# Kernel tuning notes

Hardware: AMD Instinct MI355X
Metric: run time of the kernel (lower is better)

Reference implementation:

```python
import jax, jax.numpy as jnp
import numpy as np

# Model dims (match init_kwargs)
E = 2048   # embed_dim
H = 16     # num_heads
QR = 512   # q_low_rank
KVR = 512  # kv_low_rank
DR = 64    # rope_dim
DV = 128   # v_head_dim
S = 2048   # seq_len


def _make_rotary(seq_len, dim):
    inv_freq = 1.0 / jnp.power(10000.0, jnp.arange(0, dim, 2, dtype=jnp.float32) / dim)
    t = jnp.arange(seq_len, dtype=jnp.float32)
    freqs = jnp.outer(t, inv_freq)  # (S, dim//2)
    return jnp.sin(freqs), jnp.cos(freqs)


def _apply_rope(x, sin, cos):
    # x: (S, H_or_1, D); sin/cos: (S, D//2)
    d = x.shape[-1] // 2
    x1, x2 = x[..., :d], x[..., d:]
    s = jnp.concatenate([sin, sin], axis=-1)[:, None, :]
    c = jnp.concatenate([cos, cos], axis=-1)[:, None, :]
    return x * c + jnp.concatenate([-x2, x1], axis=-1) * s


def setup_inputs() -> dict:
    key = jax.random.key(0)
    ks = jax.random.split(key, 8)
    def lin(k, out_dim, in_dim):
        return jax.random.normal(k, (out_dim, in_dim), dtype=jnp.float32) * (1.0 / np.sqrt(in_dim))
    return {
        "x": jax.random.normal(ks[0], (S, E), dtype=jnp.float32),
        "wq_down": lin(ks[1], QR, E),
        "wq_up": lin(ks[2], H * DV, QR),
        "wq_rope": lin(ks[3], H * DR, QR),
        "wkv_down": lin(ks[4], KVR, E),
        "wkv_up": lin(ks[5], H * 2 * DV, KVR),
        "wk_rope": lin(ks[6], DR, E),
        "wo": lin(ks[7], E, H * DV),
    }


def reference(x, wq_down, wq_up, wq_rope, wkv_down, wkv_up, wk_rope, wo):
    seq = x.shape[0]
    # Query path: low-rank bottleneck -> content + rope streams
    c_q = x @ wq_down.T                                   # (S, QR)
    q_content = (c_q @ wq_up.T).reshape(seq, H, DV)       # (S, H, DV)
    q_rope = (c_q @ wq_rope.T).reshape(seq, H, DR)        # (S, H, DR)
    # KV path: shared low-rank bottleneck
    c_kv = x @ wkv_down.T                                 # (S, KVR)
    kv = c_kv @ wkv_up.T                                  # (S, 2*H*DV)
    k_content_flat, v_flat = jnp.split(kv, 2, axis=-1)
    k_content = k_content_flat.reshape(seq, H, DV)
    v = v_flat.reshape(seq, H, DV)
    # Shared key-RoPE projection (one per position, broadcast over heads)
    k_rope_shared = (x @ wk_rope.T)[:, None, :]           # (S, 1, DR)
    sin, cos = _make_rotary(seq, DR)
    q_rope_rot = _apply_rope(q_rope, sin, cos)            # (S, H, DR)
    k_rope_rot = _apply_rope(k_rope_shared, sin, cos)     # (S, 1, DR)
    # Concat content + rope streams; QK head dim = DV + DR
    dt = jnp.bfloat16
    q = jnp.concatenate([q_content, q_rope_rot], axis=-1).astype(dt)                            # (S, H, DV+DR)
    k = jnp.concatenate([k_content, jnp.broadcast_to(k_rope_rot, (seq, H, DR))], axis=-1).astype(dt)
    v_attn = v.astype(dt)
    scale = 1.0 / np.sqrt(DV + DR)
    # Attention. Note: original zero-pads V to DV+DR then slices output back to
    # DV -- mathematically identical to attending with unpadded V.
    logits = jnp.einsum('shd,thd->hst', q, k).astype(jnp.float32) * scale  # (H, S, S)
    probs = jax.nn.softmax(logits, axis=-1).astype(dt)
    attn = jnp.einsum('hst,thd->shd', probs, v_attn)      # (S, H, DV)
    attn_flat = attn.reshape(seq, H * DV)
    return (attn_flat @ wo.T).astype(jnp.float32)         # (S, E)
```

## Files before the change

kernel.cpp:

```cpp
#include <hip/hip_runtime.h>
#include <stdint.h>
#include <math.h>

#define S_LEN 2048
#define NH 16

typedef __attribute__((ext_vector_type(8))) short bf16x8;
typedef __attribute__((ext_vector_type(4))) float f32x4;
typedef __attribute__((ext_vector_type(16))) float f32x16;
typedef unsigned short ush;

__device__ __forceinline__ ush f2bf(float f) {
  union { float f; unsigned u; } v; v.f = f;
  unsigned x = v.u;
  return (ush)((x + 0x7fffu + ((x >> 16) & 1u)) >> 16);
}
__device__ __forceinline__ float bf2f(ush b) {
  union { unsigned u; float f; } v; v.u = ((unsigned)b) << 16;
  return v.f;
}
__device__ __forceinline__ ush f2h(float f) {
  _Float16 h = (_Float16)f;
  union { _Float16 h; ush u; } v; v.h = h;
  return v.u;
}
__device__ __forceinline__ float h2f(ush u) {
  union { ush u; _Float16 h; } v; v.u = u;
  return (float)v.h;
}

__device__ __forceinline__ void gload_lds16(const ush* g, ush* l) {
  __builtin_amdgcn_global_load_lds((const __attribute__((address_space(1))) void*)g,
                                   (__attribute__((address_space(3))) void*)l, 16, 0, 0);
}

__global__ void mega_pack(const float* __restrict__ wq_down, const float* __restrict__ wkv_down,
                          const float* __restrict__ wk_rope, const float* __restrict__ wq_up,
                          const float* __restrict__ wq_rope, const float* __restrict__ wkv_up,
                          const float* __restrict__ wo, const float* __restrict__ x,
                          ush* __restrict__ wdh, ush* __restrict__ wqh, ush* __restrict__ wkvuh,
                          ush* __restrict__ woh, ush* __restrict__ xh, float* __restrict__ tab) {
  int idx = blockIdx.x * 256 + threadIdx.x;
  if (idx < 3604480) {
    int qi = idx * 4;
    if (qi < 2359296) {
      int r = qi >> 11, c = qi & 2047;
      float4 v = {0.f, 0.f, 0.f, 0.f};
      if (r < 512)       v = *(const float4*)(wq_down + (size_t)r * 2048 + c);
      else if (r < 1024) v = *(const float4*)(wkv_down + (size_t)(r - 512) * 2048 + c);
      else if (r < 1088) v = *(const float4*)(wk_rope + (size_t)(r - 1024) * 2048 + c);
      ushort4 o4; o4.x = f2h(v.x); o4.y = f2h(v.y); o4.z = f2h(v.z); o4.w = f2h(v.w);
      *(ushort4*)(wdh + qi) = o4;
      return;
    }
    qi -= 2359296;
    if (qi < 1572864) {
      int r = qi >> 9, c = qi & 511;
      const float* src = (r < 2048) ? wq_up + (size_t)r * 512 + c
                                    : wq_rope + (size_t)(r - 2048) * 512 + c;
      float4 v = *(const float4*)src;
      ushort4 o4; o4.x = f2h(v.x); o4.y = f2h(v.y); o4.z = f2h(v.z); o4.w = f2h(v.w);
      *(ushort4*)(wqh + qi) = o4;
      return;
    }
    qi -= 1572864;
    if (qi < 2097152) {
      float4 v = *(const float4*)(wkv_up + qi);
      ushort4 o4; o4.x = f2h(v.x); o4.y = f2h(v.y); o4.z = f2h(v.z); o4.w = f2h(v.w);
      *(ushort4*)(wkvuh + qi) = o4;
      return;
    }
    qi -= 2097152;
    if (qi < 4194304) {
      float4 v = *(const float4*)(wo + qi);
      ushort4 o4; o4.x = f2h(v.x); o4.y = f2h(v.y); o4.z = f2h(v.z); o4.w = f2h(v.w);
      *(ushort4*)(woh + qi) = o4;
      return;
    }
    qi -= 4194304;
    {
      float4 v = *(const float4*)(x + qi);
      ushort4 o4; o4.x = f2h(v.x); o4.y = f2h(v.y); o4.z = f2h(v.z); o4.w = f2h(v.w);
      *(ushort4*)(xh + qi) = o4;
      return;
    }
  }
  idx -= 3604480;
  if (idx < 65536) {
    int tt = idx >> 5, i = idx & 31;
    float inv_freq = 1.0f / powf(10000.0f, (float)i * (1.0f / 32.0f));
    float fr = (float)tt * inv_freq;
    tab[idx] = sinf(fr);
    tab[65536 + idx] = cosf(fr);
  }
}

__global__ __launch_bounds__(256) void gemm_down(
    const ush* __restrict__ A, const ush* __restrict__ B,
    ush* __restrict__ cqh, ush* __restrict__ ckvh, float* __restrict__ krl) {
  constexpr int BM = 128, BN = 64, K = 2048, FI = 4, FJ = 2;
  __shared__ __align__(16) ush As[2 * BM * 32];
  __shared__ __align__(16) ush Bs[2 * BN * 32];
  const int t = threadIdx.x, l = t & 63, w = t >> 6;
  const int wm = w & 1, wn = w >> 1;
  const int m0 = blockIdx.y * BM, n0 = blockIdx.x * BN;
  const int lm = l & 15, lq = l >> 4;
  const int lr = l >> 2, lc = (l & 3) * 8;

  f32x4 acc[FI][FJ];
  const f32x4 zero = {0.f, 0.f, 0.f, 0.f};
#pragma unroll
  for (int i = 0; i < FI; i++)
#pragma unroll
    for (int j = 0; j < FJ; j++) acc[i][j] = zero;

  const ush* Ag[2];
#pragma unroll
  for (int i = 0; i < 2; i++) Ag[i] = A + (size_t)(m0 + w * 32 + i * 16 + lr) * K + lc;
  const ush* Bg = B + (size_t)(n0 + w * 16 + lr) * K + lc;

#pragma unroll
  for (int i = 0; i < 2; i++) gload_lds16(Ag[i], As + w * 1024 + i * 512);
  gload_lds16(Bg, Bs + w * 512);

  int cur = 0;
  for (int k0 = 0; k0 < K; k0 += 32) {
    asm volatile("s_waitcnt vmcnt(0)" ::: "memory");
    __builtin_amdgcn_s_barrier();
    __builtin_amdgcn_sched_barrier(0);
    if (k0 + 32 < K) {
      int nb = cur ^ 1;
#pragma unroll
      for (int i = 0; i < 2; i++)
        gload_lds16(Ag[i] + k0 + 32, As + nb * 4096 + w * 1024 + i * 512);
      gload_lds16(Bg + k0 + 32, Bs + nb * 2048 + w * 512);
    }
    __builtin_amdgcn_sched_barrier(0);
    const ush* Asc = As + cur * 4096;
    const ush* Bsc = Bs + cur * 2048;
    bf16x8 af[FI], bfr[FJ];
#pragma unroll
    for (int i = 0; i < FI; i++)
      af[i] = *(const bf16x8*)(Asc + (wm * 64 + i * 16 + lm) * 32 + lq * 8);
#pragma unroll
    for (int j = 0; j < FJ; j++)
      bfr[j] = *(const bf16x8*)(Bsc + (wn * 32 + j * 16 + lm) * 32 + lq * 8);
#pragma unroll
    for (int i = 0; i < FI; i++)
#pragma unroll
      for (int j = 0; j < FJ; j++)
        acc[i][j] = __builtin_amdgcn_mfma_f32_16x16x32_f16(af[i], bfr[j], acc[i][j], 0, 0, 0);
    cur ^= 1;
  }

#pragma unroll
  for (int i = 0; i < FI; i++)
#pragma unroll
    for (int j = 0; j < FJ; j++)
#pragma unroll
      for (int r = 0; r < 4; r++) {
        int mm = m0 + wm * 64 + i * 16 + lq * 4 + r;
        int nn = n0 + wn * 32 + j * 16 + lm;
        float v = acc[i][j][r];
        if (nn < 512)       cqh[(size_t)mm * 512 + nn] = f2h(v);
        else if (nn < 1024) ckvh[(size_t)mm * 512 + nn - 512] = f2h(v);
        else if (nn < 1088) krl[(size_t)mm * 64 + nn - 1024] = v;
      }
}

__global__ __launch_bounds__(256) void gemm_up(
    const ush* __restrict__ cqh, const ush* __restrict__ wqh,
    const ush* __restrict__ ckvh, const ush* __restrict__ wkvuh,
    ush* __restrict__ qupf, ush* __restrict__ kvf) {
  constexpr int K = 512, FI = 4, FJ = 4;
  __shared__ __align__(16) ush As[2 * 128 * 32];
  __shared__ __align__(16) ush Bs[2 * 128 * 32];
  int bx = blockIdx.x;
  const ush* A; const ush* B; ush* C; int ldc;
  if (bx < 24) { A = cqh; B = wqh; C = qupf; ldc = 3072; }
  else { bx -= 24; A = ckvh; B = wkvuh; C = kvf; ldc = 4096; }
  const int t = threadIdx.x, l = t & 63, w = t >> 6;
  const int wm = w & 1, wn = w >> 1;
  const int m0 = blockIdx.y * 128, n0 = bx * 128;
  const int lm = l & 15, lq = l >> 4;
  const int lr = l >> 2, lc = (l & 3) * 8;

  f32x4 acc[FI][FJ];
  const f32x4 zero = {0.f, 0.f, 0.f, 0.f};
#pragma unroll
  for (int i = 0; i < FI; i++)
#pragma unroll
    for (int j = 0; j < FJ; j++) acc[i][j] = zero;

  const ush* Ag[2]; const ush* Bg[2];
#pragma unroll
  for (int i = 0; i < 2; i++) {
    Ag[i] = A + (size_t)(m0 + w * 32 + i * 16 + lr) * K + lc;
    Bg[i] = B + (size_t)(n0 + w * 32 + i * 16 + lr) * K + lc;
  }

#pragma unroll
  for (int i = 0; i < 2; i++) {
    gload_lds16(Ag[i], As + w * 1024 + i * 512);
    gload_lds16(Bg[i], Bs + w * 1024 + i * 512);
  }

  int cur = 0;
  for (int k0 = 0; k0 < K; k0 += 32) {
    asm volatile("s_waitcnt vmcnt(0)" ::: "memory");
    __builtin_amdgcn_s_barrier();
    __builtin_amdgcn_sched_barrier(0);
    if (k0 + 32 < K) {
      int nb = cur ^ 1;
#pragma unroll
      for (int i = 0; i < 2; i++) {
        gload_lds16(Ag[i] + k0 + 32, As + nb * 4096 + w * 1024 + i * 512);
        gload_lds16(Bg[i] + k0 + 32, Bs + nb * 4096 + w * 1024 + i * 512);
      }
    }
    __builtin_amdgcn_sched_barrier(0);
    const ush* Asc = As + cur * 4096;
    const ush* Bsc = Bs + cur * 4096;
    bf16x8 af[FI], bfr[FJ];
#pragma unroll
    for (int i = 0; i < FI; i++)
      af[i] = *(const bf16x8*)(Asc + (wm * 64 + i * 16 + lm) * 32 + lq * 8);
#pragma unroll
    for (int j = 0; j < FJ; j++)
      bfr[j] = *(const bf16x8*)(Bsc + (wn * 64 + j * 16 + lm) * 32 + lq * 8);
#pragma unroll
    for (int i = 0; i < FI; i++)
#pragma unroll
      for (int j = 0; j < FJ; j++)
        acc[i][j] = __builtin_amdgcn_mfma_f32_16x16x32_f16(af[i], bfr[j], acc[i][j], 0, 0, 0);
    cur ^= 1;
  }

#pragma unroll
  for (int i = 0; i < FI; i++)
#pragma unroll
    for (int j = 0; j < FJ; j++)
#pragma unroll
      for (int r = 0; r < 4; r++) {
        int mm = m0 + wm * 64 + i * 16 + lq * 4 + r;
        int nn = n0 + wn * 64 + j * 16 + lm;
        C[(size_t)mm * ldc + nn] = f2h(acc[i][j][r]);
      }
}

__global__ __launch_bounds__(256) void gemm_out(
    const ush* __restrict__ A, const ush* __restrict__ B, float* __restrict__ C,
    int K, int ldc) {
  constexpr int BM = 128, BN = 64, FI = 4, FJ = 2;
  __shared__ __align__(16) ush As[2 * BM * 32];
  __shared__ __align__(16) ush Bs[2 * BN * 32];
  const int t = threadIdx.x, l = t & 63, w = t >> 6;
  const int wm = w & 1, wn = w >> 1;
  const int m0 = blockIdx.y * BM, n0 = blockIdx.x * BN;
  const int lm = l & 15, lq = l >> 4;
  const int lr = l >> 2, lc = (l & 3) * 8;

  f32x4 acc[FI][FJ];
  const f32x4 zero = {0.f, 0.f, 0.f, 0.f};
#pragma unroll
  for (int i = 0; i < FI; i++)
#pragma unroll
    for (int j = 0; j < FJ; j++) acc[i][j] = zero;

  const ush* Ag[2];
#pragma unroll
  for (int i = 0; i < 2; i++) Ag[i] = A + (size_t)(m0 + w * 32 + i * 16 + lr) * K + lc;
  const ush* Bg = B + (size_t)(n0 + w * 16 + lr) * K + lc;

#pragma unroll
  for (int i = 0; i < 2; i++) gload_lds16(Ag[i], As + w * 1024 + i * 512);
  gload_lds16(Bg, Bs + w * 512);

  int cur = 0;
  for (int k0 = 0; k0 < K; k0 += 32) {
    asm volatile("s_waitcnt vmcnt(0)" ::: "memory");
    __builtin_amdgcn_s_barrier();
    __builtin_amdgcn_sched_barrier(0);
    if (k0 + 32 < K) {
      int nb = cur ^ 1;
#pragma unroll
      for (int i = 0; i < 2; i++)
        gload_lds16(Ag[i] + k0 + 32, As + nb * 4096 + w * 1024 + i * 512);
      gload_lds16(Bg + k0 + 32, Bs + nb * 2048 + w * 512);
    }
    __builtin_amdgcn_sched_barrier(0);
    const ush* Asc = As + cur * 4096;
    const ush* Bsc = Bs + cur * 2048;
    bf16x8 af[FI], bfr[FJ];
#pragma unroll
    for (int i = 0; i < FI; i++)
      af[i] = *(const bf16x8*)(Asc + (wm * 64 + i * 16 + lm) * 32 + lq * 8);
#pragma unroll
    for (int j = 0; j < FJ; j++)
      bfr[j] = *(const bf16x8*)(Bsc + (wn * 32 + j * 16 + lm) * 32 + lq * 8);
#pragma unroll
    for (int i = 0; i < FI; i++)
#pragma unroll
      for (int j = 0; j < FJ; j++)
        acc[i][j] = __builtin_amdgcn_mfma_f32_16x16x32_f16(af[i], bfr[j], acc[i][j], 0, 0, 0);
    cur ^= 1;
  }

#pragma unroll
  for (int i = 0; i < FI; i++)
#pragma unroll
    for (int j = 0; j < FJ; j++)
#pragma unroll
      for (int r = 0; r < 4; r++) {
        int mm = m0 + wm * 64 + i * 16 + lq * 4 + r;
        int nn = n0 + wn * 32 + j * 16 + lm;
        C[(size_t)mm * ldc + nn] = acc[i][j][r];
      }
}

__global__ void build_all(const ush* __restrict__ qupf, const ush* __restrict__ kvf,
                          const float* __restrict__ krl, const float* __restrict__ tab,
                          ush* __restrict__ qb, ush* __restrict__ kbt, ush* __restrict__ vtt) {
  const float scale = 0.07216878364870323f;
  if (blockIdx.x >= 6272) {
    __shared__ ush Vt[128 * 72];
    int b = blockIdx.x - 6272;
    const int T = b & 31, h = b >> 5, t = threadIdx.x;
    const int key = t >> 5, d0 = (t & 31) * 4;
#pragma unroll
    for (int pass = 0; pass < 8; ++pass) {
      int k = key + pass * 8;
      int s = T * 64 + k;
      ushort4 v = *(const ushort4*)(kvf + (size_t)s * 4096 + 2048 + h * 128 + d0);
      Vt[(d0 + 0) * 72 + k] = f2bf(h2f(v.x));
      Vt[(d0 + 1) * 72 + k] = f2bf(h2f(v.y));
      Vt[(d0 + 2) * 72 + k] = f2bf(h2f(v.z));
      Vt[(d0 + 3) * 72 + k] = f2bf(h2f(v.w));
    }
    __syncthreads();
    ush* dst = vtt + (size_t)(h * 32 + T) * 9216;
    for (int off = t; off < 1152; off += 256) {
      int row = off / 9, c8 = (off % 9) * 8;
      *(bf16x8*)(dst + row * 72 + c8) = *(const bf16x8*)(Vt + row * 72 + c8);
    }
    return;
  }
  int idx = blockIdx.x * 256 + threadIdx.x;
  if (idx < 786432) {
    int g = idx % 24; int sh = idx / 24; int h = sh & 15; int s = sh >> 4;
    int d0 = g * 8;
    union { ush u[8]; bf16x8 v; } out;
    if (d0 < 128) {
      bf16x8 src = *(const bf16x8*)(qupf + (size_t)s * 3072 + h * 128 + d0);
#pragma unroll
      for (int e = 0; e < 8; e++) out.u[e] = f2bf(h2f((ush)src[e]) * scale);
    } else {
      int r = d0 - 128;
      int i0 = r & 31;
      const ush* qr = qupf + (size_t)s * 3072 + 2048 + h * 64;
      bf16x8 xv = *(const bf16x8*)(qr + r);
      bf16x8 ov = (r < 32) ? *(const bf16x8*)(qr + r + 32) : *(const bf16x8*)(qr + r - 32);
      float4 sn0 = *(const float4*)(tab + s * 32 + i0);
      float4 sn1 = *(const float4*)(tab + s * 32 + i0 + 4);
      float4 cs0 = *(const float4*)(tab + 65536 + s * 32 + i0);
      float4 cs1 = *(const float4*)(tab + 65536 + s * 32 + i0 + 4);
      float sn[8] = {sn0.x, sn0.y, sn0.z, sn0.w, sn1.x, sn1.y, sn1.z, sn1.w};
      float cs[8] = {cs0.x, cs0.y, cs0.z, cs0.w, cs1.x, cs1.y, cs1.z, cs1.w};
#pragma unroll
      for (int e = 0; e < 8; e++) {
        float x = h2f((ush)xv[e]);
        float other = (r < 32) ? -h2f((ush)ov[e]) : h2f((ush)ov[e]);
        out.u[e] = f2bf((x * cs[e] + other * sn[e]) * scale);
      }
    }
    *(bf16x8*)(qb + ((size_t)h * S_LEN + s) * 192 + d0) = out.v;
    return;
  }
  idx -= 786432;
  {
    int g = idx % 25; int row = idx / 25;
    int key = row & 63; int r3 = row >> 6; int T = r3 & 31; int h = r3 >> 5;
    int s = T * 64 + key;
    int c0 = g * 8;
    union { ush u[8]; bf16x8 v; } out;
    if (c0 < 128) {
      bf16x8 src = *(const bf16x8*)(kvf + (size_t)s * 4096 + h * 128 + c0);
#pragma unroll
      for (int e = 0; e < 8; e++) out.u[e] = f2bf(h2f((ush)src[e]));
    } else if (c0 < 192) {
      int r = c0 - 128;
      int i0 = r & 31;
      const float* kr = krl + (size_t)s * 64;
      float4 xv0 = *(const float4*)(kr + r);
      float4 xv1 = *(const float4*)(kr + r + 4);
      const float* kro = (r < 32) ? kr + r + 32 : kr + r - 32;
      float4 ov0 = *(const float4*)(kro);
      float4 ov1 = *(const float4*)(kro + 4);
      float4 sn0 = *(const float4*)(tab + s * 32 + i0);
      float4 sn1 = *(const float4*)(tab + s * 32 + i0 + 4);
      float4 cs0 = *(const float4*)(tab + 65536 + s * 32 + i0);
      float4 cs1 = *(const float4*)(tab + 65536 + s * 32 + i0 + 4);
      float xv[8] = {xv0.x, xv0.y, xv0.z, xv0.w, xv1.x, xv1.y, xv1.z, xv1.w};
      float ov[8] = {ov0.x, ov0.y, ov0.z, ov0.w, ov1.x, ov1.y, ov1.z, ov1.w};
      float sn[8] = {sn0.x, sn0.y, sn0.z, sn0.w, sn1.x, sn1.y, sn1.z, sn1.w};
      float cs[8] = {cs0.x, cs0.y, cs0.z, cs0.w, cs1.x, cs1.y, cs1.z, cs1.w};
#pragma unroll
      for (int e = 0; e < 8; e++) {
        float other = (r < 32) ? -ov[e] : ov[e];
        out.u[e] = f2bf(xv[e] * cs[e] + other * sn[e]);
      }
    } else {
#pragma unroll
      for (int e = 0; e < 8; e++) out.u[e] = 0;
    }
    *(bf16x8*)(kbt + ((size_t)(h * 32 + T) * 64 + key) * 200 + c0) = out.v;
  }
}

__global__ __launch_bounds__(512, 2) void attn_fused(
    const ush* __restrict__ qb, const ush* __restrict__ kbt, const ush* __restrict__ vtt,
    ush* __restrict__ opart, float* __restrict__ ml) {
  __shared__ __align__(16) ush Ks[2][64 * 200];
  __shared__ __align__(16) ush Vs[2][128 * 72];
  const int t = threadIdx.x, l = t & 63, w = t >> 6;
  const int id = blockIdx.x + 8 * (blockIdx.y + 16 * blockIdx.z);
  const int wid = (id & 7) * 32 + (id >> 3);
  const int qx = wid & 7, h = (wid >> 3) & 15, z = wid >> 7;
  const int qrow0 = qx * 256 + w * 32;
  const int ln = l & 31, lh = l >> 5;

  bf16x8 qf[12];
#pragma unroll
  for (int st = 0; st < 12; st++)
    qf[st] = *(const bf16x8*)(qb + ((size_t)h * S_LEN + qrow0 + ln) * 192 + st * 16 + lh * 8);
#pragma unroll
  for (int st = 0; st < 12; st++) asm volatile("" : "+v"(qf[st]));

  f32x16 o[4];
#pragma unroll
  for (int i = 0; i < 4; i++)
#pragma unroll
    for (int r = 0; r < 16; r++) o[i][r] = 0.f;
  float ps = 0.f;

  const ush* kbase = kbt + (size_t)(h * 32 + z * 16) * 12800;
  const ush* vbase = vtt + (size_t)(h * 32 + z * 16) * 9216;

  auto smpack = [&ps](const f32x16& svv, bf16x8& f0, bf16x8& f1) {
    unsigned pk8[8];
#pragma unroll
    for (int g = 0; g < 4; g++) {
      float p0 = __expf(svv[4 * g + 0]);
      float p1 = __expf(svv[4 * g + 1]);
      float p2 = __expf(svv[4 * g + 2]);
      float p3 = __expf(svv[4 * g + 3]);
      ps += (p0 + p1) + (p2 + p3);
      unsigned lo, hi;
      asm("v_cvt_pk_bf16_f32 %0, %1, %2" : "=v"(lo) : "v"(p0), "v"(p1));
      asm("v_cvt_pk_bf16_f32 %0, %1, %2" : "=v"(hi) : "v"(p2), "v"(p3));
      pk8[2 * g] = lo; pk8[2 * g + 1] = hi;
    }
    asm("v_permlane32_swap_b32 %0, %1" : "+v"(pk8[0]), "+v"(pk8[2]));
    asm("v_permlane32_swap_b32 %0, %1" : "+v"(pk8[1]), "+v"(pk8[3]));
    asm("v_permlane32_swap_b32 %0, %1" : "+v"(pk8[4]), "+v"(pk8[6]));
    asm("v_permlane32_swap_b32 %0, %1" : "+v"(pk8[5]), "+v"(pk8[7]));
    union { unsigned d[4]; bf16x8 v; } u0, u1;
    u0.d[0] = pk8[0]; u0.d[1] = pk8[1]; u0.d[2] = pk8[2]; u0.d[3] = pk8[3];
    u1.d[0] = pk8[4]; u1.d[1] = pk8[5]; u1.d[2] = pk8[6]; u1.d[3] = pk8[7];
    f0 = u0.v; f1 = u1.v;
  };

  for (int c = w; c < 43; c += 8) {
    if (c < 25) gload_lds16(kbase + c * 512 + l * 8, &Ks[0][c * 512]);
    else        gload_lds16(vbase + (c - 25) * 512 + l * 8, &Vs[0][(c - 25) * 512]);
  }

  int cur = 0;
  for (int it = 0; it < 16; ++it) {
    asm volatile("s_waitcnt vmcnt(0)" ::: "memory");
    __builtin_amdgcn_s_barrier();
    __builtin_amdgcn_sched_barrier(0);
    if (it < 15) {
      const ush* ksrc = kbase + (size_t)(it + 1) * 12800;
      const ush* vsrc = vbase + (size_t)(it + 1) * 9216;
      ush* kd = &Ks[cur ^ 1][0];
      ush* vd = &Vs[cur ^ 1][0];
      for (int c = w; c < 43; c += 8) {
        if (c < 25) gload_lds16(ksrc + c * 512 + l * 8, kd + c * 512);
        else        gload_lds16(vsrc + (c - 25) * 512 + l * 8, vd + (c - 25) * 512);
      }
    }
    __builtin_amdgcn_sched_barrier(0);

    const ush* Kb = &Ks[cur][0];
    const ush* Vb = &Vs[cur][0];

    f32x16 sv0, sv1;
#pragma unroll
    for (int r = 0; r < 16; r++) { sv0[r] = 0.f; sv1[r] = 0.f; }

    __builtin_amdgcn_s_setprio(1);
#pragma unroll
    for (int st = 0; st < 12; st++) {
      bf16x8 af = *(const bf16x8*)(Kb + ln * 200 + st * 16 + lh * 8);
      sv0 = __builtin_amdgcn_mfma_f32_32x32x16_bf16(af, qf[st], sv0, 0, 0, 0);
    }
    __builtin_amdgcn_s_setprio(0);

    bf16x8 pf00, pf01;
    smpack(sv0, pf00, pf01);

    __builtin_amdgcn_s_setprio(1);
#pragma unroll
    for (int st = 0; st < 12; st++) {
      bf16x8 af = *(const bf16x8*)(Kb + (32 + ln) * 200 + st * 16 + lh * 8);
      sv1 = __builtin_amdgcn_mfma_f32_32x32x16_bf16(af, qf[st], sv1, 0, 0, 0);
    }
    __builtin_amdgcn_s_setprio(0);

    __builtin_amdgcn_s_setprio(1);
#pragma unroll
    for (int db = 0; db < 4; db++) {
      bf16x8 vf0 = *(const bf16x8*)(Vb + (db * 32 + ln) * 72 + lh * 8);
      bf16x8 vf1 = *(const bf16x8*)(Vb + (db * 32 + ln) * 72 + 16 + lh * 8);
      o[db] = __builtin_amdgcn_mfma_f32_32x32x16_bf16(vf0, pf00, o[db], 0, 0, 0);
      o[db] = __builtin_amdgcn_mfma_f32_32x32x16_bf16(vf1, pf01, o[db], 0, 0, 0);
    }
    __builtin_amdgcn_s_setprio(0);

    bf16x8 pf10, pf11;
    smpack(sv1, pf10, pf11);

    __builtin_amdgcn_s_setprio(1);
#pragma unroll
    for (int db = 0; db < 4; db++) {
      bf16x8 vf0 = *(const bf16x8*)(Vb + (db * 32 + ln) * 72 + 32 + lh * 8);
      bf16x8 vf1 = *(const bf16x8*)(Vb + (db * 32 + ln) * 72 + 48 + lh * 8);
      o[db] = __builtin_amdgcn_mfma_f32_32x32x16_bf16(vf0, pf10, o[db], 0, 0, 0);
      o[db] = __builtin_amdgcn_mfma_f32_32x32x16_bf16(vf1, pf11, o[db], 0, 0, 0);
    }
    __builtin_amdgcn_s_setprio(0);

    cur ^= 1;
  }

  float lsum = ps + __shfl_xor(ps, 32, 64);
  const int s = qrow0 + ln;
  const size_t rbase = ((size_t)((z * 16 + h) * 2048) + s) * 128;
#pragma unroll
  for (int db = 0; db < 4; db++)
#pragma unroll
    for (int rq = 0; rq < 4; rq++) {
      ushort4 v4;
      v4.x = f2h(o[db][rq * 4 + 0] * 0.0625f);
      v4.y = f2h(o[db][rq * 4 + 1] * 0.0625f);
      v4.z = f2h(o[db][rq * 4 + 2] * 0.0625f);
      v4.w = f2h(o[db][rq * 4 + 3] * 0.0625f);
      *(ushort4*)(&opart[rbase + db * 32 + 8 * rq + 4 * lh]) = v4;
    }
  if (lh == 0) ml[(size_t)(z * 16 + h) * 2048 + s] = lsum;
}

__global__ __launch_bounds__(256) void attn_reduce(const ush* __restrict__ opart,
                                                   const float* __restrict__ ml,
                                                   ush* __restrict__ attnh) {
  int row = blockIdx.x * 8 + (threadIdx.x >> 5);
  int lane = threadIdx.x & 31;
  int h = row >> 11, s = row & 2047;
  float lsum = 0.f;
#pragma unroll
  for (int z = 0; z < 2; z++) lsum += ml[(size_t)(z * 16 + h) * 2048 + s];
  float inv = 16.0f / lsum;
  int c = lane * 4;
  float a[4] = {0.f, 0.f, 0.f, 0.f};
#pragma unroll
  for (int z = 0; z < 2; z++) {
    ushort4 v = *(const ushort4*)(&opart[((size_t)(z * 16 + h) * 2048 + s) * 128 + c]);
    a[0] += h2f(v.x); a[1] += h2f(v.y); a[2] += h2f(v.z); a[3] += h2f(v.w);
  }
  ushort4 o4;
  o4.x = f2h(bf2f(f2bf(a[0] * inv)));
  o4.y = f2h(bf2f(f2bf(a[1] * inv)));
  o4.z = f2h(bf2f(f2bf(a[2] * inv)));
  o4.w = f2h(bf2f(f2bf(a[3] * inv)));
  *(ushort4*)(&attnh[(size_t)s * 2048 + h * 128 + c]) = o4;
}

extern "C" void kernel_launch(void* const* d_in, const int* in_sizes, int n_in,
                              void* d_out, int out_size, void* d_ws, size_t ws_size,
                              hipStream_t stream) {
  const float* x        = (const float*)d_in[0];
  const float* wq_down  = (const float*)d_in[1];
  const float* wq_up    = (const float*)d_in[2];
  const float* wq_rope  = (const float*)d_in[3];
  const float* wkv_down = (const float*)d_in[4];
  const float* wkv_up   = (const float*)d_in[5];
  const float* wk_rope  = (const float*)d_in[6];
  const float* wo       = (const float*)d_in[7];
  char* ws = (char*)d_ws;

  size_t off = 0;
  auto alloc = [&](size_t b) { size_t c = off; off += (b + 255) & ~(size_t)255; return c; };
  const size_t XH    = alloc(2048UL * 2048 * 2);
  const size_t WDH   = alloc(1152UL * 2048 * 2);
  const size_t KRL   = alloc(2048UL * 64 * 4);
  const size_t CQH   = alloc(2048UL * 512 * 2);
  const size_t CKVH  = alloc(2048UL * 512 * 2);
  const size_t WQH   = alloc(3072UL * 512 * 2);
  const size_t QUPF  = alloc(2048UL * 3072 * 2);
  const size_t WKVUH = alloc(4096UL * 512 * 2);
  const size_t WOH   = alloc(2048UL * 2048 * 2);
  const size_t KVF   = alloc(2048UL * 4096 * 2);
  const size_t QB    = alloc(16UL * 2048 * 192 * 2);
  const size_t KBT   = alloc(16UL * 32 * 12800 * 2);
  const size_t VTT   = alloc(16UL * 32 * 9216 * 2);
  const size_t TAB   = alloc(2048UL * 32 * 4 * 2);
  const size_t OPART = alloc(2UL * 16 * 2048 * 128 * 2);
  const size_t ML    = alloc(2UL * 16 * 2048 * 4);
  const size_t ATTNH = XH;

  mega_pack<<<dim3(14336), 256, 0, stream>>>(
      wq_down, wkv_down, wk_rope, wq_up, wq_rope, wkv_up, wo, x,
      (ush*)(ws + WDH), (ush*)(ws + WQH), (ush*)(ws + WKVUH),
      (ush*)(ws + WOH), (ush*)(ws + XH), (float*)(ws + TAB));

  gemm_down<<<dim3(18, 16), 256, 0, stream>>>(
      (ush*)(ws + XH), (ush*)(ws + WDH),
      (ush*)(ws + CQH), (ush*)(ws + CKVH), (float*)(ws + KRL));

  gemm_up<<<dim3(56, 16), 256, 0, stream>>>(
      (ush*)(ws + CQH), (ush*)(ws + WQH),
      (ush*)(ws + CKVH), (ush*)(ws + WKVUH),
      (ush*)(ws + QUPF), (ush*)(ws + KVF));

  build_all<<<dim3(6784), 256, 0, stream>>>(
      (const ush*)(ws + QUPF), (const ush*)(ws + KVF), (const float*)(ws + KRL),
      (const float*)(ws + TAB), (ush*)(ws + QB), (ush*)(ws + KBT), (ush*)(ws + VTT));

  attn_fused<<<dim3(8, 16, 2), 512, 0, stream>>>(
      (ush*)(ws + QB), (ush*)(ws + KBT), (ush*)(ws + VTT),
      (ush*)(ws + OPART), (float*)(ws + ML));
  attn_reduce<<<dim3(4096), 256, 0, stream>>>((const ush*)(ws + OPART), (const float*)(ws + ML),
                                              (ush*)(ws + ATTNH));

  gemm_out<<<dim3(32, 16), 256, 0, stream>>>(
      (ush*)(ws + ATTNH), (ush*)(ws + WOH), (float*)d_out, 2048, 2048);
}
```

Measured before the change: 270.0 us.

## Use 128x128 tiles with split-K and atomic accumulation in output projection GEMM

The output projection GEMM grows its tile from 128x64 to 128x128, so each block reuses more loaded data per MFMA. It also splits K in two along a new grid z dimension, keeping the block count at 512. Partial results are combined with float atomicAdd into the output. This depends on the output buffer being zeroed before the launch, and atomic stores cost more than plain stores.

```diff
diff --git a/kernel.cpp b/kernel.cpp
--- a/kernel.cpp
+++ b/kernel.cpp
@@ -251,12 +251,13 @@
 __global__ __launch_bounds__(256) void gemm_out(
     const ush* __restrict__ A, const ush* __restrict__ B, float* __restrict__ C,
     int K, int ldc) {
-  constexpr int BM = 128, BN = 64, FI = 4, FJ = 2;
-  __shared__ __align__(16) ush As[2 * BM * 32];
-  __shared__ __align__(16) ush Bs[2 * BN * 32];
+  constexpr int FI = 4, FJ = 4, KS = 1024;
+  __shared__ __align__(16) ush As[2 * 128 * 32];
+  __shared__ __align__(16) ush Bs[2 * 128 * 32];
   const int t = threadIdx.x, l = t & 63, w = t >> 6;
   const int wm = w & 1, wn = w >> 1;
-  const int m0 = blockIdx.y * BM, n0 = blockIdx.x * BN;
+  const int m0 = blockIdx.y * 128, n0 = blockIdx.x * 128;
+  const int kbase = blockIdx.z * KS;
   const int lm = l & 15, lq = l >> 4;
   const int lr = l >> 2, lc = (l & 3) * 8;
 
@@ -267,37 +268,42 @@
 #pragma unroll
     for (int j = 0; j < FJ; j++) acc[i][j] = zero;
 
-  const ush* Ag[2];
-#pragma unroll
-  for (int i = 0; i < 2; i++) Ag[i] = A + (size_t)(m0 + w * 32 + i * 16 + lr) * K + lc;
-  const ush* Bg = B + (size_t)(n0 + w * 16 + lr) * K + lc;
-
-#pragma unroll
-  for (int i = 0; i < 2; i++) gload_lds16(Ag[i], As + w * 1024 + i * 512);
-  gload_lds16(Bg, Bs + w * 512);
+  const ush* Ag[2]; const ush* Bg[2];
+#pragma unroll
+  for (int i = 0; i < 2; i++) {
+    Ag[i] = A + (size_t)(m0 + w * 32 + i * 16 + lr) * K + kbase + lc;
+    Bg[i] = B + (size_t)(n0 + w * 32 + i * 16 + lr) * K + kbase + lc;
+  }
+
+#pragma unroll
+  for (int i = 0; i < 2; i++) {
+    gload_lds16(Ag[i], As + w * 1024 + i * 512);
+    gload_lds16(Bg[i], Bs + w * 1024 + i * 512);
+  }
 
   int cur = 0;
-  for (int k0 = 0; k0 < K; k0 += 32) {
+  for (int k0 = 0; k0 < KS; k0 += 32) {
     asm volatile("s_waitcnt vmcnt(0)" ::: "memory");
     __builtin_amdgcn_s_barrier();
     __builtin_amdgcn_sched_barrier(0);
-    if (k0 + 32 < K) {
+    if (k0 + 32 < KS) {
       int nb = cur ^ 1;
 #pragma unroll
-      for (int i = 0; i < 2; i++)
+      for (int i = 0; i < 2; i++) {
         gload_lds16(Ag[i] + k0 + 32, As + nb * 4096 + w * 1024 + i * 512);
-      gload_lds16(Bg + k0 + 32, Bs + nb * 2048 + w * 512);
+        gload_lds16(Bg[i] + k0 + 32, Bs + nb * 4096 + w * 1024 + i * 512);
+      }
     }
     __builtin_amdgcn_sched_barrier(0);
     const ush* Asc = As + cur * 4096;
-    const ush* Bsc = Bs + cur * 2048;
+    const ush* Bsc = Bs + cur * 4096;
     bf16x8 af[FI], bfr[FJ];
 #pragma unroll
     for (int i = 0; i < FI; i++)
       af[i] = *(const bf16x8*)(Asc + (wm * 64 + i * 16 + lm) * 32 + lq * 8);
 #pragma unroll
     for (int j = 0; j < FJ; j++)
-      bfr[j] = *(const bf16x8*)(Bsc + (wn * 32 + j * 16 + lm) * 32 + lq * 8);
+      bfr[j] = *(const bf16x8*)(Bsc + (wn * 64 + j * 16 + lm) * 32 + lq * 8);
 #pragma unroll
     for (int i = 0; i < FI; i++)
 #pragma unroll
@@ -313,8 +319,8 @@
 #pragma unroll
       for (int r = 0; r < 4; r++) {
         int mm = m0 + wm * 64 + i * 16 + lq * 4 + r;
-        int nn = n0 + wn * 32 + j * 16 + lm;
-        C[(size_t)mm * ldc + nn] = acc[i][j][r];
+        int nn = n0 + wn * 64 + j * 16 + lm;
+        atomicAdd(&C[(size_t)mm * ldc + nn], acc[i][j][r]);
       }
 }
 
@@ -643,6 +649,6 @@
   attn_reduce<<<dim3(4096), 256, 0, stream>>>((const ush*)(ws + OPART), (const float*)(ws + ML),
                                               (ush*)(ws + ATTNH));
 
-  gemm_out<<<dim3(32, 16), 256, 0, stream>>>(
+  gemm_out<<<dim3(16, 16, 2), 256, 0, stream>>>(
       (ush*)(ws + ATTNH), (ush*)(ws + WOH), (float*)d_out, 2048, 2048);
 }
```

Measured after the change: 286.8 us. +6.2%, slower.
